# Optimization experiments

Measured on AMD Instinct MI355X. Metric: run time of the kernel, lower is better.

Reference implementation:

```python
import jax, jax.numpy as jnp
import numpy as np

B, C, T = 64, 8, 2048
K, DIL = 64, 1
NF = 32                      # n_frequencies (<= K//2+1 = 33)
MLP, HID = 32, 64
FFT_DIM = C * NF * 2         # 512
W = T - DIL * (K - 1)        # 1985 windows (== max_windows)


def setup_inputs() -> dict:
    key = jax.random.key(0)
    ks = jax.random.split(key, 12)
    s = 0.05
    return {
        "x": jax.random.normal(ks[0], (B, C, T), jnp.float32),
        "proj_w": jax.random.normal(ks[1], (MLP, FFT_DIM), jnp.float32) * s,
        "proj_b": jax.random.normal(ks[2], (MLP,), jnp.float32) * s,
        "w0": jax.random.normal(ks[3], (HID, MLP), jnp.float32) * s,      # Linear(32->64)
        "b0": jax.random.normal(ks[4], (HID,), jnp.float32) * s,
        "a0": jnp.ones((HID,), jnp.float32),                              # Snake a (a_init=1)
        "w1": jax.random.normal(ks[5], (MLP, HID), jnp.float32) * s,      # Linear(64->32)
        "b1": jax.random.normal(ks[6], (MLP,), jnp.float32) * s,
        "a1": jnp.ones((MLP,), jnp.float32),
        "wo": jax.random.normal(ks[7], (1, MLP), jnp.float32) * s,        # output Linear(32->1)
        "bo": jax.random.normal(ks[8], (1,), jnp.float32) * s,
        "agg": jax.random.normal(ks[9], (W,), jnp.float32) * s,           # agg_weights
    }


def _snake(x, a):
    aa = jnp.abs(a) + 1e-8
    return x + jnp.sin(aa * x) ** 2 / aa


def reference(x, proj_w, proj_b, w0, b0, a0, w1, b1, a1, wo, bo, agg):
    eff = DIL * (K - 1)
    # window t uses sorted indices t-(K-1)*DIL, ..., t  (step DIL)
    idx = eff + jnp.arange(W)[:, None] - (K - 1 - jnp.arange(K))[None, :] * DIL  # [W,K]
    win = x[:, :, idx]                                   # [B,C,W,K]
    fft = jnp.fft.rfft(win, axis=-1)[..., :NF]           # [B,C,W,NF] complex
    mag = jnp.log1p(jnp.abs(fft))
    ph = jnp.arctan2(fft.imag, fft.real) / np.pi
    feat = jnp.stack([mag, ph], axis=-1)                 # [B,C,W,NF,2]
    feat = jnp.transpose(feat, (0, 2, 1, 3, 4)).reshape(B, W, FFT_DIM)
    proj = jnp.tanh(feat @ proj_w.T + proj_b) * np.pi    # [B,W,MLP]
    h = _snake(proj @ w0.T + b0, a0)                     # [B,W,HID]
    h = _snake(h @ w1.T + b1, a1)                        # [B,W,MLP]
    out_t = (h @ wo.T + bo)[..., 0]                      # [B,W]
    wts = jax.nn.softmax(agg)                            # [W]
    return jnp.sum(out_t * wts, axis=1)                  # [B]
```

## Files before the change

kernel.cpp:

```cpp
#include <hip/hip_runtime.h>
#include <math.h>

#define B_ 64
#define C_ 8
#define T_ 2048
#define NF_ 32
#define MLP_ 32
#define HID_ 64
#define W_ 1985
#define CH_ 32
#define NCHUNK_ 63
#define PI_F 3.14159265358979323846f

typedef _Float16 f16x8 __attribute__((ext_vector_type(8)));
typedef _Float16 f16x2 __attribute__((ext_vector_type(2)));
typedef float    f32x4 __attribute__((ext_vector_type(4)));

#define WS_PARTIAL 64
#define WS_TWHI    4096
#define WS_TWLO    6144
#define WS_PWHI    8192
#define WS_PWLO    16384
#define WS_W0HI    24576
#define WS_W0LO    25600
#define WS_W1HI    26624
#define WS_W1LO    27648

__device__ __forceinline__ float fast_rcp(float x) { return __builtin_amdgcn_rcpf(x); }

__device__ __forceinline__ float fast_atan2pi(float y, float x)
{
    const float ax = fabsf(x), ay = fabsf(y);
    const float mx = fmaxf(ax, ay), mn = fminf(ax, ay);
    const float r  = mn * fast_rcp(fmaxf(mx, 1e-30f));
    const float t  = r * r;
    float a = -0.003730950f;
    a = fmaf(a, t,  0.016759940f);
    a = fmaf(a, t, -0.037059946f);
    a = fmaf(a, t,  0.061602941f);
    a = fmaf(a, t, -0.105877528f);
    a = fmaf(a, t,  0.318302656f);
    a *= r;
    a = (ay > ax) ? (0.5f - a) : a;
    a = (x < 0.0f) ? (1.0f - a) : a;
    return copysignf(a, y);
}

__device__ __forceinline__ float fast_tanh(float x)
{
    const float e = __expf(2.0f * x);
    return 1.0f - 2.0f * fast_rcp(e + 1.0f);
}

__device__ __forceinline__ float fast_snake(float h, float rcp_aa, float aa)
{
    const float s = __sinf(aa * h);
    return h + s * s * rcp_aa;
}

__device__ __forceinline__ float dot4(float4 a, float4 b, float acc)
{
    return fmaf(a.x, b.x, fmaf(a.y, b.y, fmaf(a.z, b.z, fmaf(a.w, b.w, acc))));
}

__device__ __forceinline__ unsigned packhl(float v)
{
    const _Float16 h = (_Float16)v;
    const _Float16 l = (_Float16)(v - (float)h);
    f16x2 p; p[0] = h; p[1] = l;
    return __builtin_bit_cast(unsigned, p);
}

__device__ __forceinline__ void unpack8(const unsigned* u, f16x8& ah, f16x8& al)
{
    union { unsigned w[4]; f16x8 v; } H, L;
    #pragma unroll
    for (int j = 0; j < 4; ++j) {
        H.w[j] = __builtin_amdgcn_perm(u[2*j+1], u[2*j], 0x05040100u);
        L.w[j] = __builtin_amdgcn_perm(u[2*j+1], u[2*j], 0x07060302u);
    }
    ah = H.v; al = L.v;
}

__device__ __forceinline__ void gload_lds16(const void* g, void* l)
{
    __builtin_amdgcn_global_load_lds(
        (const __attribute__((address_space(1))) void*)g,
        (__attribute__((address_space(3))) void*)l, 16, 0, 0);
}

__global__ __launch_bounds__(1024) void k_pre(
    const float* __restrict__ agg, const float* __restrict__ pw,
    const float* __restrict__ w0g, const float* __restrict__ w1g,
    float* __restrict__ ws)
{
    __shared__ float red[1024];
    const int t   = threadIdx.x;
    const int blk = blockIdx.x;

    _Float16* pwHi = (_Float16*)(ws + WS_PWHI);
    _Float16* pwLo = (_Float16*)(ws + WS_PWLO);
    #pragma unroll
    for (int e = 0; e < 2; ++e) {
        const int id = blk * 2048 + e * 1024 + t;
        const float v = pw[id];
        const _Float16 h = (_Float16)v;
        pwHi[id] = h;
        pwLo[id] = (_Float16)(v - (float)h);
    }

    if (blk != 0) return;

    _Float16* twHi = (_Float16*)(ws + WS_TWHI);
    _Float16* twLo = (_Float16*)(ws + WS_TWLO);
    #pragma unroll
    for (int e = 0; e < 4; ++e) {
        const int id = t * 4 + e;
        const int n = id >> 6, k = id & 63;
        const int f = n & 31;
        float s, c;
        sincosf(0.0981747704246810387f * (float)((k * f) & 63), &s, &c);
        const float v = (n < 32) ? c : -s;
        const _Float16 h = (_Float16)v;
        twHi[id] = h;
        twLo[id] = (_Float16)(v - (float)h);
    }

    _Float16* w0Hi = (_Float16*)(ws + WS_W0HI);
    _Float16* w0Lo = (_Float16*)(ws + WS_W0LO);
    _Float16* w1Hi = (_Float16*)(ws + WS_W1HI);
    _Float16* w1Lo = (_Float16*)(ws + WS_W1LO);
    #pragma unroll
    for (int e = 0; e < 2; ++e) {
        const int id = e * 1024 + t;
        const float v0 = w0g[id];
        const _Float16 h0 = (_Float16)v0;
        w0Hi[id] = h0;
        w0Lo[id] = (_Float16)(v0 - (float)h0);
        const float v1 = w1g[id];
        const _Float16 h1 = (_Float16)v1;
        w1Hi[id] = h1;
        w1Lo[id] = (_Float16)(v1 - (float)h1);
    }

    float m = -1e30f;
    for (int i = t; i < W_; i += 1024) m = fmaxf(m, agg[i]);
    red[t] = m;
    __syncthreads();
    for (int s = 512; s > 0; s >>= 1) {
        if (t < s) red[t] = fmaxf(red[t], red[t + s]);
        __syncthreads();
    }
    const float mx = red[0];
    __syncthreads();
    float sum = 0.f;
    for (int i = t; i < W_; i += 1024) sum += __expf(agg[i] - mx);
    red[t] = sum;
    __syncthreads();
    for (int s = 512; s > 0; s >>= 1) {
        if (t < s) red[t] += red[t + s];
        __syncthreads();
    }
    if (t == 0) { ws[0] = mx; ws[1] = red[0]; }
}

__global__ __launch_bounds__(1024, 8) void k_main(
    const float* __restrict__ x,  const float* __restrict__ pw,
    const float* __restrict__ pb, const float* __restrict__ w0g,
    const float* __restrict__ b0g,const float* __restrict__ a0g,
    const float* __restrict__ w1g,const float* __restrict__ b1g,
    const float* __restrict__ a1g,const float* __restrict__ wog,
    const float* __restrict__ bog,const float* __restrict__ agg,
    const float* __restrict__ wsp, float* __restrict__ partial)
{
    __shared__ __align__(16) _Float16 featP[16384];
    __shared__ __align__(16) _Float16 arena2[16384];
    __shared__ float smalls[260];
    __shared__ float chunkAcc[CH_];

    _Float16* featHi = featP;
    _Float16* featLo = featP + 8192;
    _Float16* twHiL  = arena2;
    _Float16* twLoL  = arena2 + 4096;
    unsigned* xtileP = (unsigned*)(arena2 + 8192);
    _Float16* pw0Hi  = arena2;
    _Float16* pw0Lo  = arena2 + 8192;
    float*    pacc   = (float*)featP;
    _Float16* projHi = featP + 8448;
    _Float16* projLo = featP + 8448 + 1280;
    _Float16* h0Hi   = featP + 11008;
    _Float16* h0Lo   = featP + 11008 + 2304;
    float*    h1L    = (float*)featP;

    const int t     = threadIdx.x;
    const int chunk = blockIdx.x;
    const int b     = blockIdx.y;
    const int w0c   = chunk * CH_;
    const int wid   = t >> 6;
    const int lane  = t & 63;
    const int m16   = lane & 15;
    const int kl    = lane >> 4;
    const int cdft  = wid >> 1;

    {
        const int gl = (wid & 7) * 64 + lane;
        const int n  = gl >> 3, q = gl & 7;
        const int srcg = n * 8 + (q ^ (n & 7));
        const float* srcbase = wsp + ((wid < 8) ? WS_TWHI : WS_TWLO);
        _Float16* dst = ((wid < 8) ? twHiL : twLoL) + gl * 8;
        gload_lds16((const char*)srcbase + srcg * 16, dst);
    }

    if (t < C_ * 96) {
        const int c = t / 96;
        const int j = t - c * 96;
        int gi = w0c + j; if (gi > T_ - 1) gi = T_ - 1;
        xtileP[c * 100 + j] = packhl(x[((size_t)b * C_ + c) * T_ + gi]);
    }
    if (t < 257) {
        float smv;
        if      (t <  32) smv = pb[t];
        else if (t <  96) smv = b0g[t - 32];
        else if (t < 160) smv = a0g[t - 96];
        else if (t < 192) smv = b1g[t - 160];
        else if (t < 224) smv = a1g[t - 192];
        else if (t < 256) smv = wog[t - 224];
        else              smv = bog[0];
        smalls[t] = smv;
    }
    __syncthreads();

    f32x4 dacc0 = {0.f,0.f,0.f,0.f}, dacc1 = {0.f,0.f,0.f,0.f};
    f32x4 dacc2 = {0.f,0.f,0.f,0.f}, dacc3 = {0.f,0.f,0.f,0.f};
    const int wra = (wid & 1) * 16 + m16;
    {
        #pragma unroll
        for (int kstep = 0; kstep < 2; ++kstep) {
            const int kq = kstep * 4 + kl;
            unsigned ut[8];
            #pragma unroll
            for (int j = 0; j < 8; ++j) ut[j] = xtileP[cdft * 100 + wra + kq * 8 + j];
            f16x8 ah, al; unpack8(ut, ah, al);
            f32x4* dp[4] = { &dacc0, &dacc1, &dacc2, &dacc3 };
            #pragma unroll
            for (int nt = 0; nt < 4; ++nt) {
                const int nrow = nt * 16 + m16;
                const int gB = (nrow * 8 + (kq ^ (nrow & 7))) * 8;
                const f16x8 bh = *(const f16x8*)&twHiL[gB];
                const f16x8 bl = *(const f16x8*)&twLoL[gB];
                f32x4 a = *dp[nt];
                a = __builtin_amdgcn_mfma_f32_16x16x32_f16(ah, bh, a, 0, 0, 0);
                a = __builtin_amdgcn_mfma_f32_16x16x32_f16(al, bh, a, 0, 0, 0);
                a = __builtin_amdgcn_mfma_f32_16x16x32_f16(ah, bl, a, 0, 0, 0);
                *dp[nt] = a;
            }
        }
    }
    __syncthreads();

    {
        const char* pwbytes = (const char*)wsp;
        #pragma unroll
        for (int r = 0; r < 2; ++r) {
            const int gw = (r * 16 + wid) * 64;
            const int g  = gw + lane;
            const int plane = g >> 10;
            const int gp = g & 1023;
            const int o  = gp >> 5;
            const int q  = gp & 31;
            const size_t srcoff = (size_t)(plane ? WS_PWLO : WS_PWHI) * 4
                                + (size_t)o * 1024 + (size_t)((q ^ (o & 7)) * 16);
            gload_lds16(pwbytes + srcoff, (char*)arena2 + (size_t)g * 16);
        }
    }

    unsigned heldHi[2][4], heldLo[2][4];
    {
        const int wbase = (wid & 1) * 16 + kl * 4;
        const int ccl   = cdft & 3;
        const float reA[2][4] = {{dacc0[0],dacc0[1],dacc0[2],dacc0[3]},
                                 {dacc1[0],dacc1[1],dacc1[2],dacc1[3]}};
        const float imA[2][4] = {{dacc2[0],dacc2[1],dacc2[2],dacc2[3]},
                                 {dacc3[0],dacc3[1],dacc3[2],dacc3[3]}};
        #pragma unroll
        for (int fi = 0; fi < 2; ++fi) {
            const int f = fi * 16 + m16;
            const int g = ccl * 8 + (f >> 2);
            const int sub = 2 * (f & 3);
            #pragma unroll
            for (int r = 0; r < 4; ++r) {
                const int w  = wbase + r;
                const float re = reA[fi][r], im = imA[fi][r];
                const float mag = __logf(1.0f + __builtin_amdgcn_sqrtf(re*re + im*im));
                const float ph  = fast_atan2pi(im, re);
                const _Float16 mh = (_Float16)mag;
                const _Float16 qh = (_Float16)ph;
                f16x2 vh; vh[0] = mh; vh[1] = qh;
                f16x2 vl;
                vl[0] = (_Float16)(mag - (float)mh);
                vl[1] = (_Float16)(ph  - (float)qh);
                if (wid < 8) {
                    const int off = w * 256 + ((g ^ (w & 7)) * 8) + sub;
                    *(f16x2*)&featHi[off] = vh;
                    *(f16x2*)&featLo[off] = vl;
                } else {
                    heldHi[fi][r] = __builtin_bit_cast(unsigned, vh);
                    heldLo[fi][r] = __builtin_bit_cast(unsigned, vl);
                }
            }
        }
    }
    __syncthreads();

    const _Float16* pwHi = (const _Float16*)(wsp + WS_PWHI);
    const _Float16* pwLo = (const _Float16*)(wsp + WS_PWLO);
    {
        const int wt = (wid >> 1) & 1;
        const int ot = wid & 1;
        const int kq4 = wid >> 2;
        const int arow = wt * 16 + m16;
        const int brow = ot * 16 + m16;
        f32x4 acc = {0.f, 0.f, 0.f, 0.f};
        #pragma unroll
        for (int p = 0; p < 2; ++p) {
            #pragma unroll
            for (int kstep = 0; kstep < 2; ++kstep) {
                const int kp = kq4 * 64 + kstep * 32 + kl * 8;
                f16x8 bh, bl;
                if (p == 0) {
                    const int offB = brow * 256 + (((kp >> 3) ^ (brow & 7)) * 8);
                    bh = *(const f16x8*)&pw0Hi[offB];
                    bl = *(const f16x8*)&pw0Lo[offB];
                } else {
                    bh = *(const f16x8*)&pwHi[(size_t)brow * 512 + 256 + kp];
                    bl = *(const f16x8*)&pwLo[(size_t)brow * 512 + 256 + kp];
                }
                const int g0 = kp >> 3;
                const int offA = arow * 256 + ((g0 ^ (arow & 7)) * 8);
                const f16x8 ah = *(const f16x8*)&featHi[offA];
                const f16x8 al = *(const f16x8*)&featLo[offA];
                acc = __builtin_amdgcn_mfma_f32_16x16x32_f16(ah, bh, acc, 0, 0, 0);
                acc = __builtin_amdgcn_mfma_f32_16x16x32_f16(al, bh, acc, 0, 0, 0);
                acc = __builtin_amdgcn_mfma_f32_16x16x32_f16(ah, bl, acc, 0, 0, 0);
            }
            if (p == 0) {
                __syncthreads();
                if (wid >= 8) {
                    const int wbase = (wid & 1) * 16 + kl * 4;
                    const int ccl   = cdft & 3;
                    #pragma unroll
                    for (int fi = 0; fi < 2; ++fi) {
                        const int f = fi * 16 + m16;
                        const int g = ccl * 8 + (f >> 2);
                        const int sub = 2 * (f & 3);
                        #pragma unroll
                        for (int r = 0; r < 4; ++r) {
                            const int w  = wbase + r;
                            const int off = w * 256 + ((g ^ (w & 7)) * 8) + sub;
                            *(unsigned*)&featHi[off] = heldHi[fi][r];
                            *(unsigned*)&featLo[off] = heldLo[fi][r];
                        }
                    }
                }
                __syncthreads();
            }
        }
        __syncthreads();
        #pragma unroll
        for (int r = 0; r < 4; ++r) {
            const int w = wt * 16 + kl * 4 + r;
            const int o = ot * 16 + m16;
            pacc[kq4 * 1056 + w * 33 + o] = acc[r];
        }
    }
    __syncthreads();

    {
        const int o = t & 31;
        const int w = t >> 5;
        float s = smalls[o];
        #pragma unroll
        for (int q = 0; q < 4; ++q) s += pacc[q * 1056 + w * 33 + o];
        const float pr = fast_tanh(s) * PI_F;
        const _Float16 h = (_Float16)pr;
        projHi[w * 40 + o] = h;
        projLo[w * 40 + o] = (_Float16)(pr - (float)h);
    }
    __syncthreads();

    const _Float16* w0Hi = (const _Float16*)(wsp + WS_W0HI);
    const _Float16* w0Lo = (const _Float16*)(wsp + WS_W0LO);
    if (wid < 8) {
        const int wt = wid & 1;
        const int ot = wid >> 1;
        const int arow = wt * 16 + m16;
        const int brow = ot * 16 + m16;
        const f16x8 ah = *(const f16x8*)&projHi[arow * 40 + kl * 8];
        const f16x8 al = *(const f16x8*)&projLo[arow * 40 + kl * 8];
        const f16x8 bh = *(const f16x8*)&w0Hi[brow * 32 + kl * 8];
        const f16x8 bl = *(const f16x8*)&w0Lo[brow * 32 + kl * 8];
        f32x4 acc = {0.f, 0.f, 0.f, 0.f};
        acc = __builtin_amdgcn_mfma_f32_16x16x32_f16(ah, bh, acc, 0, 0, 0);
        acc = __builtin_amdgcn_mfma_f32_16x16x32_f16(al, bh, acc, 0, 0, 0);
        acc = __builtin_amdgcn_mfma_f32_16x16x32_f16(ah, bl, acc, 0, 0, 0);
        const int o  = ot * 16 + m16;
        const float b0v = smalls[32 + o];
        const float aa  = fabsf(smalls[96 + o]) + 1e-8f;
        const float ra  = fast_rcp(aa);
        #pragma unroll
        for (int r = 0; r < 4; ++r) {
            const int w = wt * 16 + kl * 4 + r;
            const float hv = fast_snake(acc[r] + b0v, ra, aa);
            const _Float16 h = (_Float16)hv;
            h0Hi[w * 72 + o] = h;
            h0Lo[w * 72 + o] = (_Float16)(hv - (float)h);
        }
    }
    __syncthreads();

    const _Float16* w1Hi = (const _Float16*)(wsp + WS_W1HI);
    const _Float16* w1Lo = (const _Float16*)(wsp + WS_W1LO);
    if (wid < 4) {
        const int wt = wid & 1;
        const int ot = wid >> 1;
        const int arow = wt * 16 + m16;
        const int brow = ot * 16 + m16;
        f32x4 acc = {0.f, 0.f, 0.f, 0.f};
        #pragma unroll
        for (int ks = 0; ks < 2; ++ks) {
            const f16x8 ah = *(const f16x8*)&h0Hi[arow * 72 + ks * 32 + kl * 8];
            const f16x8 al = *(const f16x8*)&h0Lo[arow * 72 + ks * 32 + kl * 8];
            const f16x8 bh = *(const f16x8*)&w1Hi[brow * 64 + ks * 32 + kl * 8];
            const f16x8 bl = *(const f16x8*)&w1Lo[brow * 64 + ks * 32 + kl * 8];
            acc = __builtin_amdgcn_mfma_f32_16x16x32_f16(ah, bh, acc, 0, 0, 0);
            acc = __builtin_amdgcn_mfma_f32_16x16x32_f16(al, bh, acc, 0, 0, 0);
            acc = __builtin_amdgcn_mfma_f32_16x16x32_f16(ah, bl, acc, 0, 0, 0);
        }
        const int o  = ot * 16 + m16;
        const float b1v = smalls[160 + o];
        const float aa  = fabsf(smalls[192 + o]) + 1e-8f;
        const float ra  = fast_rcp(aa);
        #pragma unroll
        for (int r = 0; r < 4; ++r) {
            const int w = wt * 16 + kl * 4 + r;
            h1L[w * 36 + o] = fast_snake(acc[r] + b1v, ra, aa);
        }
    }
    __syncthreads();

    if (t < CH_) {
        const int w = t;
        float acc = 0.f;
        #pragma unroll
        for (int q = 0; q < 8; ++q)
            acc = dot4(*(const float4*)&h1L[w * 36 + q * 4],
                       *(const float4*)&smalls[224 + q * 4], acc);
        const float val = acc + smalls[256];
        const int wg = w0c + w;
        const float sw = (wg < W_) ? __expf(agg[wg] - wsp[0]) / wsp[1] : 0.f;
        chunkAcc[w] = val * sw;
    }
    __syncthreads();

    if (t < 32) {
        float vs = chunkAcc[t];
        vs += __shfl_down(vs, 16);
        vs += __shfl_down(vs, 8);
        vs += __shfl_down(vs, 4);
        vs += __shfl_down(vs, 2);
        vs += __shfl_down(vs, 1);
        if (t == 0) partial[(size_t)chunk * B_ + b] = vs;
    }
}

__global__ void k_reduce(const float* __restrict__ partial, float* __restrict__ out)
{
    const int b = threadIdx.x;
    if (b < B_) {
        float s = 0.f;
        for (int c = 0; c < NCHUNK_; ++c) s += partial[(size_t)c * B_ + b];
        out[b] = s;
    }
}

extern "C" void kernel_launch(void* const* d_in, const int* in_sizes, int n_in,
                              void* d_out, int out_size, void* d_ws, size_t ws_size,
                              hipStream_t stream)
{
    const float* x   = (const float*)d_in[0];
    const float* pw  = (const float*)d_in[1];
    const float* pb  = (const float*)d_in[2];
    const float* w0  = (const float*)d_in[3];
    const float* b0  = (const float*)d_in[4];
    const float* a0  = (const float*)d_in[5];
    const float* w1  = (const float*)d_in[6];
    const float* b1  = (const float*)d_in[7];
    const float* a1  = (const float*)d_in[8];
    const float* wo  = (const float*)d_in[9];
    const float* bo  = (const float*)d_in[10];
    const float* agg = (const float*)d_in[11];
    float* ws  = (float*)d_ws;
    float* out = (float*)d_out;

    k_pre<<<8, 1024, 0, stream>>>(agg, pw, w0, w1, ws);
    dim3 grid(NCHUNK_, B_);
    k_main<<<grid, 1024, 0, stream>>>(x, pw, pb, w0, b0, a0, w1, b1, a1, wo, bo,
                                      agg, ws, ws + WS_PARTIAL);
    k_reduce<<<1, 64, 0, stream>>>(ws + WS_PARTIAL, out);
}
```

Baseline: 112.7 us.

## Split prep kernel work across blocks, prefetch second-half weights, parallelize final reduce

The prep kernel now spreads twiddle generation, MLP weight splitting and the softmax statistics across three blocks instead of running them all serially in block 0, and uses the fast __sincosf intrinsic. In the main kernel, the global loads of the second-half projection weights are issued early, before the feature phase, so their latency overlaps other work. s_setprio is raised around the MFMA sequences. The final reduction uses 16 lanes per batch element with shuffles instead of one serial thread per batch. Together these aim to shorten the critical path of the small kernels and hide load latency, at the cost of more live registers and slightly less accurate twiddles.

Result: slower. 120.0 us (+6.5%).

```diff
diff --git a/kernel.cpp b/kernel.cpp
--- a/kernel.cpp
+++ b/kernel.cpp
@@ -109,59 +109,59 @@
         pwLo[id] = (_Float16)(v - (float)h);
     }
 
-    if (blk != 0) return;
-
-    _Float16* twHi = (_Float16*)(ws + WS_TWHI);
-    _Float16* twLo = (_Float16*)(ws + WS_TWLO);
-    #pragma unroll
-    for (int e = 0; e < 4; ++e) {
-        const int id = t * 4 + e;
-        const int n = id >> 6, k = id & 63;
-        const int f = n & 31;
-        float s, c;
-        sincosf(0.0981747704246810387f * (float)((k * f) & 63), &s, &c);
-        const float v = (n < 32) ? c : -s;
-        const _Float16 h = (_Float16)v;
-        twHi[id] = h;
-        twLo[id] = (_Float16)(v - (float)h);
-    }
-
-    _Float16* w0Hi = (_Float16*)(ws + WS_W0HI);
-    _Float16* w0Lo = (_Float16*)(ws + WS_W0LO);
-    _Float16* w1Hi = (_Float16*)(ws + WS_W1HI);
-    _Float16* w1Lo = (_Float16*)(ws + WS_W1LO);
-    #pragma unroll
-    for (int e = 0; e < 2; ++e) {
-        const int id = e * 1024 + t;
-        const float v0 = w0g[id];
-        const _Float16 h0 = (_Float16)v0;
-        w0Hi[id] = h0;
-        w0Lo[id] = (_Float16)(v0 - (float)h0);
-        const float v1 = w1g[id];
-        const _Float16 h1 = (_Float16)v1;
-        w1Hi[id] = h1;
-        w1Lo[id] = (_Float16)(v1 - (float)h1);
-    }
-
-    float m = -1e30f;
-    for (int i = t; i < W_; i += 1024) m = fmaxf(m, agg[i]);
-    red[t] = m;
-    __syncthreads();
-    for (int s = 512; s > 0; s >>= 1) {
-        if (t < s) red[t] = fmaxf(red[t], red[t + s]);
+    if (blk == 0) {
+        _Float16* twHi = (_Float16*)(ws + WS_TWHI);
+        _Float16* twLo = (_Float16*)(ws + WS_TWLO);
+        #pragma unroll
+        for (int e = 0; e < 4; ++e) {
+            const int id = t * 4 + e;
+            const int n = id >> 6, k = id & 63;
+            const int f = n & 31;
+            float s, c;
+            __sincosf(0.0981747704246810387f * (float)((k * f) & 63), &s, &c);
+            const float v = (n < 32) ? c : -s;
+            const _Float16 h = (_Float16)v;
+            twHi[id] = h;
+            twLo[id] = (_Float16)(v - (float)h);
+        }
+    } else if (blk == 1) {
+        _Float16* w0Hi = (_Float16*)(ws + WS_W0HI);
+        _Float16* w0Lo = (_Float16*)(ws + WS_W0LO);
+        _Float16* w1Hi = (_Float16*)(ws + WS_W1HI);
+        _Float16* w1Lo = (_Float16*)(ws + WS_W1LO);
+        #pragma unroll
+        for (int e = 0; e < 2; ++e) {
+            const int id = e * 1024 + t;
+            const float v0 = w0g[id];
+            const _Float16 h0 = (_Float16)v0;
+            w0Hi[id] = h0;
+            w0Lo[id] = (_Float16)(v0 - (float)h0);
+            const float v1 = w1g[id];
+            const _Float16 h1 = (_Float16)v1;
+            w1Hi[id] = h1;
+            w1Lo[id] = (_Float16)(v1 - (float)h1);
+        }
+    } else if (blk == 2) {
+        float m = -1e30f;
+        for (int i = t; i < W_; i += 1024) m = fmaxf(m, agg[i]);
+        red[t] = m;
         __syncthreads();
-    }
-    const float mx = red[0];
-    __syncthreads();
-    float sum = 0.f;
-    for (int i = t; i < W_; i += 1024) sum += __expf(agg[i] - mx);
-    red[t] = sum;
-    __syncthreads();
-    for (int s = 512; s > 0; s >>= 1) {
-        if (t < s) red[t] += red[t + s];
+        for (int s = 512; s > 0; s >>= 1) {
+            if (t < s) red[t] = fmaxf(red[t], red[t + s]);
+            __syncthreads();
+        }
+        const float mx = red[0];
         __syncthreads();
-    }
-    if (t == 0) { ws[0] = mx; ws[1] = red[0]; }
+        float sum = 0.f;
+        for (int i = t; i < W_; i += 1024) sum += __expf(agg[i] - mx);
+        red[t] = sum;
+        __syncthreads();
+        for (int s = 512; s > 0; s >>= 1) {
+            if (t < s) red[t] += red[t + s];
+            __syncthreads();
+        }
+        if (t == 0) { ws[0] = mx; ws[1] = red[0]; }
+    }
 }
 
 __global__ __launch_bounds__(1024, 8) void k_main(
@@ -230,6 +230,12 @@
     }
     __syncthreads();
 
+    const int gwt = (wid >> 1) & 1;
+    const int got = wid & 1;
+    const int gkq = wid >> 2;
+    const int garow = gwt * 16 + m16;
+    const int gbrow = got * 16 + m16;
+
     f32x4 dacc0 = {0.f,0.f,0.f,0.f}, dacc1 = {0.f,0.f,0.f,0.f};
     f32x4 dacc2 = {0.f,0.f,0.f,0.f}, dacc3 = {0.f,0.f,0.f,0.f};
     const int wra = (wid & 1) * 16 + m16;
@@ -241,19 +247,21 @@
             #pragma unroll
             for (int j = 0; j < 8; ++j) ut[j] = xtileP[cdft * 100 + wra + kq * 8 + j];
             f16x8 ah, al; unpack8(ut, ah, al);
-            f32x4* dp[4] = { &dacc0, &dacc1, &dacc2, &dacc3 };
-            #pragma unroll
-            for (int nt = 0; nt < 4; ++nt) {
-                const int nrow = nt * 16 + m16;
-                const int gB = (nrow * 8 + (kq ^ (nrow & 7))) * 8;
-                const f16x8 bh = *(const f16x8*)&twHiL[gB];
-                const f16x8 bl = *(const f16x8*)&twLoL[gB];
-                f32x4 a = *dp[nt];
-                a = __builtin_amdgcn_mfma_f32_16x16x32_f16(ah, bh, a, 0, 0, 0);
-                a = __builtin_amdgcn_mfma_f32_16x16x32_f16(al, bh, a, 0, 0, 0);
-                a = __builtin_amdgcn_mfma_f32_16x16x32_f16(ah, bl, a, 0, 0, 0);
-                *dp[nt] = a;
-            }
+            __builtin_amdgcn_s_setprio(1);
+            #define DFT_NT(dn, NT) { \
+                const int nrow = (NT) * 16 + m16; \
+                const int gB = (nrow * 8 + (kq ^ (nrow & 7))) * 8; \
+                const f16x8 bh = *(const f16x8*)&twHiL[gB]; \
+                const f16x8 bl = *(const f16x8*)&twLoL[gB]; \
+                dn = __builtin_amdgcn_mfma_f32_16x16x32_f16(ah, bh, dn, 0, 0, 0); \
+                dn = __builtin_amdgcn_mfma_f32_16x16x32_f16(al, bh, dn, 0, 0, 0); \
+                dn = __builtin_amdgcn_mfma_f32_16x16x32_f16(ah, bl, dn, 0, 0, 0); }
+            DFT_NT(dacc0, 0)
+            DFT_NT(dacc1, 1)
+            DFT_NT(dacc2, 2)
+            DFT_NT(dacc3, 3)
+            #undef DFT_NT
+            __builtin_amdgcn_s_setprio(0);
         }
     }
     __syncthreads();
@@ -272,6 +280,16 @@
                                 + (size_t)o * 1024 + (size_t)((q ^ (o & 7)) * 16);
             gload_lds16(pwbytes + srcoff, (char*)arena2 + (size_t)g * 16);
         }
+    }
+
+    const _Float16* pwHi = (const _Float16*)(wsp + WS_PWHI);
+    const _Float16* pwLo = (const _Float16*)(wsp + WS_PWLO);
+    f16x8 b1h[2], b1l[2];
+    #pragma unroll
+    for (int kstep = 0; kstep < 2; ++kstep) {
+        const int kp = gkq * 64 + kstep * 32 + kl * 8;
+        b1h[kstep] = *(const f16x8*)&pwHi[(size_t)gbrow * 512 + 256 + kp];
+        b1l[kstep] = *(const f16x8*)&pwLo[(size_t)gbrow * 512 + 256 + kp];
     }
 
     unsigned heldHi[2][4], heldLo[2][4];
@@ -312,37 +330,32 @@
     }
     __syncthreads();
 
-    const _Float16* pwHi = (const _Float16*)(wsp + WS_PWHI);
-    const _Float16* pwLo = (const _Float16*)(wsp + WS_PWLO);
     {
-        const int wt = (wid >> 1) & 1;
-        const int ot = wid & 1;
-        const int kq4 = wid >> 2;
-        const int arow = wt * 16 + m16;
-        const int brow = ot * 16 + m16;
         f32x4 acc = {0.f, 0.f, 0.f, 0.f};
         #pragma unroll
         for (int p = 0; p < 2; ++p) {
+            __builtin_amdgcn_s_setprio(1);
             #pragma unroll
             for (int kstep = 0; kstep < 2; ++kstep) {
-                const int kp = kq4 * 64 + kstep * 32 + kl * 8;
+                const int kp = gkq * 64 + kstep * 32 + kl * 8;
                 f16x8 bh, bl;
                 if (p == 0) {
-                    const int offB = brow * 256 + (((kp >> 3) ^ (brow & 7)) * 8);
+                    const int offB = gbrow * 256 + (((kp >> 3) ^ (gbrow & 7)) * 8);
                     bh = *(const f16x8*)&pw0Hi[offB];
                     bl = *(const f16x8*)&pw0Lo[offB];
                 } else {
-                    bh = *(const f16x8*)&pwHi[(size_t)brow * 512 + 256 + kp];
-                    bl = *(const f16x8*)&pwLo[(size_t)brow * 512 + 256 + kp];
+                    bh = b1h[kstep];
+                    bl = b1l[kstep];
                 }
                 const int g0 = kp >> 3;
-                const int offA = arow * 256 + ((g0 ^ (arow & 7)) * 8);
+                const int offA = garow * 256 + ((g0 ^ (garow & 7)) * 8);
                 const f16x8 ah = *(const f16x8*)&featHi[offA];
                 const f16x8 al = *(const f16x8*)&featLo[offA];
                 acc = __builtin_amdgcn_mfma_f32_16x16x32_f16(ah, bh, acc, 0, 0, 0);
                 acc = __builtin_amdgcn_mfma_f32_16x16x32_f16(al, bh, acc, 0, 0, 0);
                 acc = __builtin_amdgcn_mfma_f32_16x16x32_f16(ah, bl, acc, 0, 0, 0);
             }
+            __builtin_amdgcn_s_setprio(0);
             if (p == 0) {
                 __syncthreads();
                 if (wid >= 8) {
@@ -368,9 +381,9 @@
         __syncthreads();
         #pragma unroll
         for (int r = 0; r < 4; ++r) {
-            const int w = wt * 16 + kl * 4 + r;
-            const int o = ot * 16 + m16;
-            pacc[kq4 * 1056 + w * 33 + o] = acc[r];
+            const int w = gwt * 16 + kl * 4 + r;
+            const int o = got * 16 + m16;
+            pacc[gkq * 1056 + w * 33 + o] = acc[r];
         }
     }
     __syncthreads();
@@ -473,14 +486,23 @@
     }
 }
 
-__global__ void k_reduce(const float* __restrict__ partial, float* __restrict__ out)
-{
-    const int b = threadIdx.x;
-    if (b < B_) {
-        float s = 0.f;
-        for (int c = 0; c < NCHUNK_; ++c) s += partial[(size_t)c * B_ + b];
-        out[b] = s;
-    }
+__global__ __launch_bounds__(1024) void k_reduce(
+    const float* __restrict__ partial, float* __restrict__ out)
+{
+    const int t = threadIdx.x;
+    const int b = t >> 4;
+    const int j = t & 15;
+    float s = 0.f;
+    #pragma unroll
+    for (int q = 0; q < 4; ++q) {
+        const int c = j + q * 16;
+        if (c < NCHUNK_) s += partial[(size_t)c * B_ + b];
+    }
+    s += __shfl_xor(s, 8, 16);
+    s += __shfl_xor(s, 4, 16);
+    s += __shfl_xor(s, 2, 16);
+    s += __shfl_xor(s, 1, 16);
+    if (j == 0) out[b] = s;
 }
 
 extern "C" void kernel_launch(void* const* d_in, const int* in_sizes, int n_in,
@@ -506,5 +528,5 @@
     dim3 grid(NCHUNK_, B_);
     k_main<<<grid, 1024, 0, stream>>>(x, pw, pb, w0, b0, a0, w1, b1, a1, wo, bo,
                                       agg, ws, ws + WS_PARTIAL);
-    k_reduce<<<1, 64, 0, stream>>>(ws + WS_PARTIAL, out);
-}
+    k_reduce<<<1, 1024, 0, stream>>>(ws + WS_PARTIAL, out);
+}
```
